# Optimization experiments

Hardware: AMD Instinct MI355X
Metric: run time of the kernel (lower is better)

## Reference

```python
import jax, jax.numpy as jnp
import numpy as np

D_MODEL = 512
N_HEAD = 8
D_HEAD = 64
N_LAYER = 4
D_INNER = 2048
IN_CH = 2048
N_CLS = 64
B, T = 2, 2048
LN_EPS = 1e-5


def layer_norm(x, s, b):
    mu = jnp.mean(x, axis=-1, keepdims=True)
    var = jnp.mean(jnp.square(x - mu), axis=-1, keepdims=True)
    return (x - mu) * jax.lax.rsqrt(var + LN_EPS) * s + b


def rel_shift(x):
    # x: [q, k, b, n] -> Transformer-XL relative shift
    q, k, b, n = x.shape
    zp = jnp.zeros((q, 1, b, n), x.dtype)
    x = jnp.concatenate([zp, x], axis=1)          # [q, k+1, b, n]
    x = x.reshape(k + 1, q, b, n)[1:]             # drop first row
    return x.reshape(q, k, b, n)


def setup_inputs() -> dict:
    key = jax.random.key(0)
    ks = jax.random.split(key, 12)
    s = 0.02
    return {
        "x": jax.random.normal(ks[0], (B, IN_CH, T), jnp.float32),
        "emb_w": jax.random.normal(ks[1], (D_MODEL, IN_CH), jnp.float32) * s,
        "emb_b": jnp.zeros((D_MODEL,), jnp.float32),
        "r_w_bias": jax.random.normal(ks[2], (N_HEAD, D_HEAD), jnp.float32) * s,
        "r_r_bias": jax.random.normal(ks[3], (N_HEAD, D_HEAD), jnp.float32) * s,
        "qkv_w": jax.random.normal(ks[4], (N_LAYER, 3 * N_HEAD * D_HEAD, D_MODEL), jnp.float32) * s,
        "qkv_b": jnp.zeros((N_LAYER, 3 * N_HEAD * D_HEAD), jnp.float32),
        "r_proj_w": jax.random.normal(ks[5], (N_LAYER, N_HEAD * D_HEAD, D_MODEL), jnp.float32) * s,
        "o_w": jax.random.normal(ks[6], (N_LAYER, D_MODEL, N_HEAD * D_HEAD), jnp.float32) * s,
        "ln1_s": jnp.ones((N_LAYER, D_MODEL), jnp.float32),
        "ln1_b": jnp.zeros((N_LAYER, D_MODEL), jnp.float32),
        "ff1_w": jax.random.normal(ks[7], (N_LAYER, D_INNER, D_MODEL), jnp.float32) * s,
        "ff1_b": jnp.zeros((N_LAYER, D_INNER), jnp.float32),
        "ff2_w": jax.random.normal(ks[8], (N_LAYER, D_MODEL, D_INNER), jnp.float32) * s,
        "ff2_b": jnp.zeros((N_LAYER, D_MODEL), jnp.float32),
        "ln2_s": jnp.ones((N_LAYER, D_MODEL), jnp.float32),
        "ln2_b": jnp.zeros((N_LAYER, D_MODEL), jnp.float32),
        "cls_w": jax.random.normal(ks[9], (N_CLS, D_MODEL), jnp.float32) * s,
        "cls_b": jnp.zeros((N_CLS,), jnp.float32),
    }


def reference(x, emb_w, emb_b, r_w_bias, r_r_bias, qkv_w, qkv_b, r_proj_w, o_w,
              ln1_s, ln1_b, ff1_w, ff1_b, ff2_w, ff2_b, ln2_s, ln2_b, cls_w, cls_b):
    b, _, t = x.shape
    d = D_MODEL
    # 1x1 conv embedding, then to [T, B, d_model] layout as in _forward
    h = jnp.einsum('dc,bct->tbd', emb_w, x) + emb_b

    # sinusoidal positional embedding over pos_seq = klen-1 .. 0 (klen == qlen, mem_len=0)
    pos_seq = jnp.arange(t - 1, -1, -1, dtype=h.dtype)
    inv_freq = 1.0 / (10000.0 ** (jnp.arange(0, d, 2, dtype=h.dtype) / d))
    sinusoid = pos_seq[:, None] * inv_freq[None, :]
    pos_emb = jnp.concatenate([jnp.sin(sinusoid), jnp.cos(sinusoid)], axis=-1)  # [T, d]

    scale = 1.0 / (D_HEAD ** 0.5)
    for i in range(N_LAYER):
        w = h
        heads = jnp.einsum('ed,tbd->tbe', qkv_w[i], w) + qkv_b[i]          # [T,B,3*H*Dh]
        q, k, v = jnp.split(heads, 3, axis=-1)
        q = q.reshape(t, b, N_HEAD, D_HEAD)
        k = k.reshape(t, b, N_HEAD, D_HEAD)
        v = v.reshape(t, b, N_HEAD, D_HEAD)
        r_head_k = jnp.einsum('ed,td->te', r_proj_w[i], pos_emb).reshape(t, N_HEAD, D_HEAD)

        AC = jnp.einsum('ibnd,jbnd->ijbn', q + r_w_bias, k)                # content term
        BD = rel_shift(jnp.einsum('ibnd,jnd->ijbn', q + r_r_bias, r_head_k))  # position term
        attn_prob = jax.nn.softmax((AC + BD) * scale, axis=1)              # softmax over keys
        attn_vec = jnp.einsum('ijbn,jbnd->ibnd', attn_prob, v).reshape(t, b, N_HEAD * D_HEAD)
        attn_out = jnp.einsum('de,tbe->tbd', o_w[i], attn_vec)             # o_net (no bias)
        h = layer_norm(w + attn_out, ln1_s[i], ln1_b[i])                   # post-lnorm

        ff = jnp.einsum('fd,tbd->tbf', ff1_w[i], h) + ff1_b[i]
        ff = jax.nn.relu(ff)
        ff = jnp.einsum('df,tbf->tbd', ff2_w[i], ff) + ff2_b[i]
        h = layer_norm(h + ff, ln2_s[i], ln2_b[i])

    # 1x1 conv classifier -> [B, num_classes, T]
    out = jnp.einsum('kd,tbd->bkt', cls_w, h) + cls_b[None, :, None]
    return out
```

## Files before the change

### kernel.cpp

```cpp
#include <hip/hip_runtime.h>
#include <hip/hip_bf16.h>
#include <math.h>


#define T_   2048
#define B_   2
#define DM   512
#define NH   8
#define DH   64
#define DI   2048
#define INCH 2048
#define NCLS 64
#define MT   4096

typedef __attribute__((ext_vector_type(8))) short short8;
typedef __attribute__((ext_vector_type(4))) float float4v;

#define QSCALE 0.1803368801111204f

__device__ inline ushort f2bf(float f) {
  uint u = __float_as_uint(f);
  return (ushort)((u + 0x7FFFu + ((u >> 16) & 1u)) >> 16);
}
__device__ inline float bf2f(ushort h) { return __uint_as_float(((uint)h) << 16); }
__device__ inline uint pkbf(float a, float b) {
  __hip_bfloat162 h = __float22bfloat162_rn(float2{a, b});
  return *(uint*)&h;
}
__device__ inline void gload16(const void* g, void* lds) {
  __builtin_amdgcn_global_load_lds(
      (const __attribute__((address_space(1))) void*)g,
      (__attribute__((address_space(3))) void*)lds, 16, 0, 0);
}

__global__ __launch_bounds__(256) void pos_kernel(ushort* __restrict__ pe) {
  int idx = blockIdx.x * 256 + threadIdx.x;
  if (idx >= T_ * DM) return;
  int t = idx >> 9;
  int i = idx & 511;
  int j = (i < 256) ? i : (i - 256);
  double invf = exp(-(double)(2 * j) * (9.210340371976184 / 512.0));
  double a = (double)(T_ - 1 - t) * invf;
  pe[idx] = f2bf((i < 256) ? (float)sin(a) : (float)cos(a));
}

__global__ __launch_bounds__(256) void cvt6_kernel(
    const float* s0, ushort* d0, int n0,
    const float* s1, ushort* d1, int n1,
    const float* s2, ushort* d2, int n2,
    const float* s3, ushort* d3, int n3,
    const float* s4, ushort* d4, int n4,
    const float* s5, ushort* d5, int n5)
{
  const float* s; ushort* d; int n;
  switch (blockIdx.y) {
    case 0: s = s0; d = d0; n = n0; break;
    case 1: s = s1; d = d1; n = n1; break;
    case 2: s = s2; d = d2; n = n2; break;
    case 3: s = s3; d = d3; n = n3; break;
    case 4: s = s4; d = d4; n = n4; break;
    default: s = s5; d = d5; n = n5; break;
  }
  int i = blockIdx.x * 256 + threadIdx.x;
  if (i >= n) return;
  float4 v = ((const float4*)s)[i];
  ushort4 w = { f2bf(v.x), f2bf(v.y), f2bf(v.z), f2bf(v.w) };
  ((ushort4*)d)[i] = w;
}

__global__ __launch_bounds__(256) void xpose_kernel(const float* __restrict__ x,
                                                    ushort* __restrict__ xb) {
  __shared__ float s[32][33];
  int t0 = blockIdx.x * 32, k0 = blockIdx.y * 32, b = blockIdx.z;
  int tx = threadIdx.x & 31, ty = threadIdx.x >> 5;
#pragma unroll
  for (int l = 0; l < 4; ++l) {
    int k = k0 + ty + l * 8;
    s[ty + l * 8][tx] = x[((size_t)b * INCH + k) * T_ + t0 + tx];
  }
  __syncthreads();
#pragma unroll
  for (int l = 0; l < 4; ++l) {
    int t = t0 + ty + l * 8;
    xb[((size_t)(t * 2 + b)) * INCH + k0 + tx] = f2bf(s[tx][ty + l * 8]);
  }
}

__global__ __launch_bounds__(256) void vtrans_kernel(const ushort* __restrict__ heads,
                                                     ushort* __restrict__ vtg) {
  __shared__ ushort s[64][72];
  const int tid = threadIdx.x;
  int t0 = blockIdx.x * 64;
  int b = blockIdx.y & 1, n = blockIdx.y >> 1;
  for (int e = tid; e < 512; e += 256) {
    int r = e >> 3, c = e & 7;
    *(uint4*)&s[r][c * 8] =
        *(const uint4*)&heads[(size_t)((t0 + r) * 2 + b) * 1536 + 1024 + n * 64 + c * 8];
  }
  __syncthreads();
  for (int e = tid; e < 512; e += 256) {
    int d = e >> 3, c = e & 7;
    ushort tmp[8];
#pragma unroll
    for (int j = 0; j < 8; ++j) tmp[j] = s[c * 8 + j][d];
    *(uint4*)&vtg[((size_t)((b * 8 + n) * 64 + d)) * (size_t)T_ + t0 + c * 8] = *(uint4*)tmp;
  }
}

template<int TM, int OUTMODE, bool RELU>
__global__ __launch_bounds__(256) void gemm_bf16(
    const ushort* __restrict__ A, const ushort* __restrict__ W,
    const float* __restrict__ bias, float* __restrict__ Cf, ushort* __restrict__ Cb,
    int M, int N, int K)
{
  __shared__ __attribute__((aligned(16))) ushort As[TM * 64];
  __shared__ __attribute__((aligned(16))) ushort Bs[128 * 64];
  const int NI = TM / 32;
  const int tid  = threadIdx.x;
  const int wave = tid >> 6, lane = tid & 63;
  const int quad = lane >> 4, lidx = lane & 15;
  const int m0 = blockIdx.y * TM, n0 = blockIdx.x * 128;
  const int r8 = lane >> 3;
  const int cs = ((lane & 7) ^ (r8 & 7)) * 8;

  float4v acc[NI * 4];
#pragma unroll
  for (int i = 0; i < NI * 4; ++i) acc[i] = (float4v){0.f, 0.f, 0.f, 0.f};

  const int wm = (wave >> 1) * (TM / 2), wn = (wave & 1) * 64;

  for (int k0 = 0; k0 < K; k0 += 64) {
    __syncthreads();
#pragma unroll
    for (int g = 0; g < TM / 32; ++g) {
      int r0 = wave * 8 + g * 32;
      gload16(A + (size_t)(m0 + r0 + r8) * K + k0 + cs, &As[r0 * 64]);
    }
#pragma unroll
    for (int g = 0; g < 4; ++g) {
      int r0 = wave * 8 + g * 32;
      gload16(W + (size_t)(n0 + r0 + r8) * K + k0 + cs, &Bs[r0 * 64]);
    }
    __syncthreads();

#pragma unroll
    for (int kb = 0; kb < 2; ++kb) {
      short8 af[NI], bf4[4];
      const int ch = (((kb * 4 + quad) ^ (lidx & 7)) * 8);
#pragma unroll
      for (int i = 0; i < NI; ++i)
        af[i] = *(const short8*)&As[(wm + i * 16 + lidx) * 64 + ch];
#pragma unroll
      for (int j = 0; j < 4; ++j)
        bf4[j] = *(const short8*)&Bs[(wn + j * 16 + lidx) * 64 + ch];
#pragma unroll
      for (int i = 0; i < NI; ++i)
#pragma unroll
        for (int j = 0; j < 4; ++j)
          acc[i * 4 + j] = __builtin_amdgcn_mfma_f32_16x16x32_bf16(af[i], bf4[j], acc[i * 4 + j], 0, 0, 0);
    }
  }

  float bj[4];
#pragma unroll
  for (int j = 0; j < 4; ++j) bj[j] = bias ? bias[n0 + wn + j * 16 + lidx] : 0.f;
#pragma unroll
  for (int i = 0; i < NI; ++i) {
    int rbase = m0 + wm + i * 16 + quad * 4;
#pragma unroll
    for (int j = 0; j < 4; ++j) {
      int col = n0 + wn + j * 16 + lidx;
#pragma unroll
      for (int reg = 0; reg < 4; ++reg) {
        float v = acc[i * 4 + j][reg] + bj[j];
        if (RELU) v = fmaxf(v, 0.f);
        size_t off = (size_t)(rbase + reg) * N + col;
        if (OUTMODE != 1) Cf[off] = v;
        if (OUTMODE != 0) Cb[off] = f2bf(v);
      }
    }
  }
}

#define BM 128
#define BN 128
#define BK 16
#define LDT 132

__global__ __launch_bounds__(256) void gemm_f32(
    const float* __restrict__ A, const float* __restrict__ W,
    const float* __restrict__ bias, float* __restrict__ C,
    int M, int N, int K)
{
  __shared__ float Asm[BK][LDT];
  __shared__ float Wsm[BK][LDT];
  const int tid = threadIdx.x;
  const int m0 = blockIdx.y * BM;
  const int n0 = blockIdx.x * BN;
  const int row = tid >> 1;
  const int kh  = (tid & 1) * 8;
  const int ty  = tid >> 4;
  const int tx  = tid & 15;

  float acc[8][8];
#pragma unroll
  for (int i = 0; i < 8; ++i)
#pragma unroll
    for (int j = 0; j < 8; ++j) acc[i][j] = 0.f;

  for (int kt = 0; kt < K; kt += BK) {
    float a_reg[8], w_reg[8];
    {
      const float* ap = A + (size_t)(m0 + row) * K + (kt + kh);
      float4 v0 = *(const float4*)ap;
      float4 v1 = *(const float4*)(ap + 4);
      a_reg[0] = v0.x; a_reg[1] = v0.y; a_reg[2] = v0.z; a_reg[3] = v0.w;
      a_reg[4] = v1.x; a_reg[5] = v1.y; a_reg[6] = v1.z; a_reg[7] = v1.w;
    }
    {
      int nn = n0 + row;
      if (nn < N) {
        const float* wp = W + (size_t)nn * K + (kt + kh);
        float4 v0 = *(const float4*)wp;
        float4 v1 = *(const float4*)(wp + 4);
        w_reg[0] = v0.x; w_reg[1] = v0.y; w_reg[2] = v0.z; w_reg[3] = v0.w;
        w_reg[4] = v1.x; w_reg[5] = v1.y; w_reg[6] = v1.z; w_reg[7] = v1.w;
      } else {
#pragma unroll
        for (int q = 0; q < 8; ++q) w_reg[q] = 0.f;
      }
    }
    __syncthreads();
#pragma unroll
    for (int q = 0; q < 8; ++q) { Asm[kh + q][row] = a_reg[q]; Wsm[kh + q][row] = w_reg[q]; }
    __syncthreads();
#pragma unroll
    for (int k = 0; k < BK; ++k) {
      float4 a0 = *(const float4*)&Asm[k][ty * 4];
      float4 a1 = *(const float4*)&Asm[k][ty * 4 + 64];
      float4 b0 = *(const float4*)&Wsm[k][tx * 4];
      float4 b1 = *(const float4*)&Wsm[k][tx * 4 + 64];
      float av[8] = {a0.x, a0.y, a0.z, a0.w, a1.x, a1.y, a1.z, a1.w};
      float bv[8] = {b0.x, b0.y, b0.z, b0.w, b1.x, b1.y, b1.z, b1.w};
#pragma unroll
      for (int i = 0; i < 8; ++i)
#pragma unroll
        for (int j = 0; j < 8; ++j) acc[i][j] += av[i] * bv[j];
    }
  }

#pragma unroll
  for (int ih = 0; ih < 2; ++ih)
#pragma unroll
    for (int i = 0; i < 4; ++i) {
      int m = m0 + ty * 4 + ih * 64 + i;
#pragma unroll
      for (int jh = 0; jh < 2; ++jh) {
        int nn = n0 + tx * 4 + jh * 64;
        if (nn < N) {
          float4 v;
          v.x = acc[ih * 4 + i][jh * 4 + 0] + bias[nn + 0];
          v.y = acc[ih * 4 + i][jh * 4 + 1] + bias[nn + 1];
          v.z = acc[ih * 4 + i][jh * 4 + 2] + bias[nn + 2];
          v.w = acc[ih * 4 + i][jh * 4 + 3] + bias[nn + 3];
          *(float4*)&C[(size_t)m * N + nn] = v;
        }
      }
    }
}

#define GT 68

__device__ inline short8 bfrag(const char* base, int lidx, int quad, int kb) {
  return *(const short8*)(base + lidx * 128 + ((((kb << 2) + quad) ^ (lidx & 7)) << 4));
}

__global__ __launch_bounds__(256, 2) void attn_mfma_kernel(
    const ushort* __restrict__ heads, const ushort* __restrict__ rk,
    const ushort* __restrict__ vtg,
    const float* __restrict__ rwb, const float* __restrict__ rrb,
    ushort* __restrict__ avec)
{
  __shared__ __attribute__((aligned(16))) ushort Ks[64 * 64];
  __shared__ __attribute__((aligned(16))) ushort Vt[64 * 64];
  __shared__ __attribute__((aligned(16))) ushort Re[128 * 64];
  __shared__ __attribute__((aligned(16))) ushort Gbt[128 * GT];

  const int tid  = threadIdx.x;
  const int i0   = blockIdx.x * 64;
  const int b    = blockIdx.y & 1;
  const int n    = blockIdx.y >> 1;
  const int wave = tid >> 6;
  const int lane = tid & 63;
  const int quad = lane >> 4;
  const int lidx = lane & 15;
  const int r8   = lane >> 3;
  const int cs8  = ((lane & 7) ^ (r8 & 7)) * 8;
  const int bn64 = (b * 8 + n) * 64;
  const int rloc = wave * 16 + lidx;

  short8 qw[2], qr4[4][2], q4[2];
  {
    auto qfrag = [&](int row, int kb, const float* bias) -> short8 {
      short8 q;
      if (row < T_) q = *(const short8*)&heads[(size_t)(row * 2 + b) * 1536 + n * 64 + kb * 32 + quad * 8];
      else { for (int t = 0; t < 8; ++t) ((ushort*)&q)[t] = 0; }
      short8 o;
#pragma unroll
      for (int t = 0; t < 8; ++t) {
        float f = (bf2f((ushort)((ushort*)&q)[t]) + bias[n * 64 + kb * 32 + quad * 8 + t]) * QSCALE;
        ((ushort*)&o)[t] = f2bf(f);
      }
      return o;
    };
    qw[0] = qfrag(i0 + rloc, 0, rwb);
    qw[1] = qfrag(i0 + rloc, 1, rwb);
#pragma unroll
    for (int rt = 0; rt < 4; ++rt) {
      int row = i0 + rt * 16 + lidx;
      qr4[rt][0] = qfrag(row, 0, rrb); qr4[rt][1] = qfrag(row, 1, rrb);
    }
    int row4 = i0 + 64 + lidx;
    q4[0] = qfrag(row4, 0, rrb); q4[1] = qfrag(row4, 1, rrb);
  }

  int a0[4];
#pragma unroll
  for (int t = 0; t < 4; ++t)
    a0[t] = (t * 16 + quad * 4 + 63 - rloc) * GT + rloc;

  float4v oacc[4];
  float4v liacc = (float4v){0.f, 0.f, 0.f, 0.f};
#pragma unroll
  for (int dt = 0; dt < 4; ++dt) oacc[dt] = (float4v){0.f, 0.f, 0.f, 0.f};
  short8 ones8;
#pragma unroll
  for (int t = 0; t < 8; ++t) ((ushort*)&ones8)[t] = 0x3F80;

  auto stageKRe = [&](int jt) {
    int j0 = jt * 64, qmin = j0 + 1984 - i0;
#pragma unroll
    for (int half = 0; half < 2; ++half) {
      int r0 = 8 * wave + 32 * half;
      gload16(heads + (size_t)((j0 + r0 + r8) * 2 + b) * 1536 + 512 + n * 64 + cs8, &Ks[r0 * 64]);
    }
#pragma unroll
    for (int q4i = 0; q4i < 4; ++q4i) {
      int r0 = 8 * wave + 32 * q4i;
      int qh = qmin + r0 + r8;
      int p  = (qh > T_) ? (qh - T_ - 1) : ((qh == T_) ? 0 : qh);
      gload16(rk + (size_t)p * 2048 + n * 64 + cs8, &Re[r0 * 64]);
    }
  };
  auto stageV = [&](int jt) {
    int j0 = jt * 64;
#pragma unroll
    for (int half = 0; half < 2; ++half) {
      int r0 = 8 * wave + 32 * half;
      gload16(vtg + (size_t)(bn64 + r0 + r8) * (size_t)T_ + j0 + cs8, &Vt[r0 * 64]);
    }
  };
  auto fixup = [&](int jt) {
    int qmin = jt * 64 + 1984 - i0;
    int Tidx = T_ - qmin;
    if (Tidx >= 0 && Tidx < 128) {
      if (tid < 32) ((uint*)Re)[Tidx * 32 + tid] = 0u;
      __syncthreads();
    }
  };

  stageKRe(0);
  stageV(0);
  __syncthreads();
  fixup(0);

  for (int jt = 0; jt < 32; ++jt) {
    const int qmin = jt * 64 + 1984 - i0;
    const int wth  = T_ - qmin;

    float4v sv[4];
#pragma unroll
    for (int t = 0; t < 4; ++t) {
      const char* KsT = (const char*)Ks + t * 2048;
      short8 kf0 = bfrag(KsT, lidx, quad, 0);
      short8 kf1 = bfrag(KsT, lidx, quad, 1);
      float4v c = {0.f, 0.f, 0.f, 0.f};
      c = __builtin_amdgcn_mfma_f32_16x16x32_bf16(kf0, qw[0], c, 0, 0, 0);
      c = __builtin_amdgcn_mfma_f32_16x16x32_bf16(kf1, qw[1], c, 0, 0, 0);
      sv[t] = c;
    }

#pragma unroll
    for (int si = 0; si < 2; ++si) {
      const int ws = wave + si * 4;
      const int w0 = ws * 16;
      const char* ReW = (const char*)Re + w0 * 128;
      short8 rb0 = bfrag(ReW, lidx, quad, 0);
      short8 rb1 = bfrag(ReW, lidx, quad, 1);
#pragma unroll
      for (int rt = 0; rt < 4; ++rt) {
        bool need = si == 0 ? (rt >= 3 - wave) : (rt <= 3 - wave);
        if (need) {
          float4v g = {0.f, 0.f, 0.f, 0.f};
          g = __builtin_amdgcn_mfma_f32_16x16x32_bf16(qr4[rt][0], rb0, g, 0, 0, 0);
          g = __builtin_amdgcn_mfma_f32_16x16x32_bf16(qr4[rt][1], rb1, g, 0, 0, 0);
          uint2 st; st.x = pkbf(g[0], g[1]); st.y = pkbf(g[2], g[3]);
          *(uint2*)&Gbt[(w0 + lidx) * GT + rt * 16 + quad * 4] = st;
        }
      }
      if (si == 0 && wth < 63) {
        float4v g = {0.f, 0.f, 0.f, 0.f};
        g = __builtin_amdgcn_mfma_f32_16x16x32_bf16(q4[0], rb0, g, 0, 0, 0);
        g = __builtin_amdgcn_mfma_f32_16x16x32_bf16(q4[1], rb1, g, 0, 0, 0);
        if (quad == 0) Gbt[(w0 + lidx) * GT + 64] = f2bf(g[0]);
      }
    }
    __syncthreads();

    if (jt < 31) stageKRe(jt + 1);

    {
      const int cth = wth + rloc - 63;
#pragma unroll
      for (int t = 0; t < 4; ++t) {
        const int c0 = t * 16 + quad * 4;
#pragma unroll
        for (int r = 0; r < 4; ++r) {
          int ga = a0[t] + r * GT + ((c0 + r > cth) ? 1 : 0);
          sv[t][r] = exp2f(sv[t][r] + bf2f(Gbt[ga]));
        }
      }
    }

    short8 vb[4][2];
#pragma unroll
    for (int dt = 0; dt < 4; ++dt) {
      const char* VtT = (const char*)Vt + dt * 2048;
      vb[dt][0] = bfrag(VtT, lidx, quad, 0);
      vb[dt][1] = bfrag(VtT, lidx, quad, 1);
    }

    short8 af[2];
#pragma unroll
    for (int kb = 0; kb < 2; ++kb) {
      uint mm[4];
#pragma unroll
      for (int i = 0; i < 2; ++i) {
        uint e, o;
        asm("v_cvt_pk_bf16_f32 %0, %1, %2" : "=v"(e) : "v"(sv[2 * kb][2 * i]),     "v"(sv[2 * kb][2 * i + 1]));
        asm("v_cvt_pk_bf16_f32 %0, %1, %2" : "=v"(o) : "v"(sv[2 * kb + 1][2 * i]), "v"(sv[2 * kb + 1][2 * i + 1]));
        asm("v_permlane32_swap_b32 %0, %1" : "+v"(e), "+v"(o));
        asm("v_permlane16_swap_b32 %0, %1" : "+v"(e), "+v"(o));
        mm[i] = e; mm[2 + i] = o;
      }
      union { uint u[4]; short8 s; } cv;
      cv.u[0] = mm[0]; cv.u[1] = mm[1]; cv.u[2] = mm[2]; cv.u[3] = mm[3];
      af[kb] = cv.s;
    }

    __syncthreads();

    if (jt < 31) {
      stageV(jt + 1);
      fixup(jt + 1);
    }

#pragma unroll
    for (int dt = 0; dt < 4; ++dt) {
      oacc[dt] = __builtin_amdgcn_mfma_f32_16x16x32_bf16(af[0], vb[dt][0], oacc[dt], 0, 0, 0);
      oacc[dt] = __builtin_amdgcn_mfma_f32_16x16x32_bf16(af[1], vb[dt][1], oacc[dt], 0, 0, 0);
    }
    liacc = __builtin_amdgcn_mfma_f32_16x16x32_bf16(af[0], ones8, liacc, 0, 0, 0);
    liacc = __builtin_amdgcn_mfma_f32_16x16x32_bf16(af[1], ones8, liacc, 0, 0, 0);
  }

#pragma unroll
  for (int reg = 0; reg < 4; ++reg) {
    int i = i0 + wave * 16 + quad * 4 + reg;
    float li = liacc[reg];
#pragma unroll
    for (int dt = 0; dt < 4; ++dt) {
      float val = oacc[dt][reg] / li;
      avec[(size_t)(i * 2 + b) * DM + n * 64 + dt * 16 + lidx] = f2bf(val);
    }
  }
}

__global__ __launch_bounds__(256) void ln_res_kernel(
    float* __restrict__ h, ushort* __restrict__ hb, const float* __restrict__ delta,
    const float* __restrict__ s, const float* __restrict__ bb)
{
  const int m = blockIdx.x;
  const int tid = threadIdx.x;
  float* hp = h + (size_t)m * DM;
  ushort* hbp = hb + (size_t)m * DM;
  const float* dp = delta + (size_t)m * DM;
  float x0 = hp[tid] + dp[tid];
  float x1 = hp[tid + 256] + dp[tid + 256];
  float sum = x0 + x1, sq = x0 * x0 + x1 * x1;
#pragma unroll
  for (int o = 32; o > 0; o >>= 1) { sum += __shfl_down(sum, o); sq += __shfl_down(sq, o); }
  __shared__ float part[8];
  int wv = tid >> 6;
  if ((tid & 63) == 0) { part[wv * 2] = sum; part[wv * 2 + 1] = sq; }
  __syncthreads();
  float ts = part[0] + part[2] + part[4] + part[6];
  float tq = part[1] + part[3] + part[5] + part[7];
  float mu = ts * (1.f / DM);
  float var = tq * (1.f / DM) - mu * mu;
  float rs = rsqrtf(var + 1e-5f);
  float y0 = (x0 - mu) * rs * s[tid]       + bb[tid];
  float y1 = (x1 - mu) * rs * s[tid + 256] + bb[tid + 256];
  hp[tid] = y0;       hbp[tid] = f2bf(y0);
  hp[tid + 256] = y1; hbp[tid + 256] = f2bf(y1);
}

__global__ __launch_bounds__(256) void reorder_kernel(const float* __restrict__ ct,
                                                      float* __restrict__ out) {
  int idx = blockIdx.x * 256 + threadIdx.x;
  if (idx >= B_ * NCLS * T_) return;
  int t  = idx & (T_ - 1);
  int nc = (idx >> 11) & 63;
  int bb = idx >> 17;
  out[idx] = ct[(size_t)(t * B_ + bb) * NCLS + nc];
}

extern "C" void kernel_launch(void* const* d_in, const int* in_sizes, int n_in,
                              void* d_out, int out_size, void* d_ws, size_t ws_size,
                              hipStream_t stream)
{
  const float* x     = (const float*)d_in[0];
  const float* emb_w = (const float*)d_in[1];
  const float* emb_b = (const float*)d_in[2];
  const float* rwb   = (const float*)d_in[3];
  const float* rrb   = (const float*)d_in[4];
  const float* qkv_w = (const float*)d_in[5];
  const float* qkv_b = (const float*)d_in[6];
  const float* rproj = (const float*)d_in[7];
  const float* o_w   = (const float*)d_in[8];
  const float* ln1s  = (const float*)d_in[9];
  const float* ln1b  = (const float*)d_in[10];
  const float* ff1w  = (const float*)d_in[11];
  const float* ff1b  = (const float*)d_in[12];
  const float* ff2w  = (const float*)d_in[13];
  const float* ff2b  = (const float*)d_in[14];
  const float* ln2s  = (const float*)d_in[15];
  const float* ln2b  = (const float*)d_in[16];
  const float* clsw  = (const float*)d_in[17];
  const float* clsb  = (const float*)d_in[18];
  float* out = (float*)d_out;

  char* p = (char*)d_ws;
  float*  h       = (float*)p;   p += (size_t)MT * DM * 4;
  float*  tmpf    = (float*)p;   p += (size_t)MT * DM * 4;
  ushort* hb      = (ushort*)p;  p += (size_t)MT * DM * 2;
  ushort* headsb  = (ushort*)p;  p += (size_t)MT * 1536 * 2;
  ushort* peb     = (ushort*)p;  p += (size_t)T_ * DM * 2;
  ushort* rk_all  = (ushort*)p;  p += (size_t)T_ * 2048 * 2;
  ushort* avecb   = (ushort*)p;  p += (size_t)MT * DM * 2;
  ushort* xfb     = (ushort*)p;  p += (size_t)MT * INCH * 2;
  ushort* emb_wb  = (ushort*)p;  p += (size_t)DM * INCH * 2;
  ushort* qkv_wb  = (ushort*)p;  p += (size_t)4 * 1536 * DM * 2;
  ushort* rproj_wb= (ushort*)p;  p += (size_t)4 * DM * DM * 2;
  ushort* o_wb    = (ushort*)p;  p += (size_t)4 * DM * DM * 2;
  ushort* ff1_wb  = (ushort*)p;  p += (size_t)4 * DI * DM * 2;
  ushort* ff2_wb  = (ushort*)p;  p += (size_t)4 * DM * DI * 2;
  ushort* vtg     = xfb;

  cvt6_kernel<<<dim3(4096, 6), 256, 0, stream>>>(
      emb_w, emb_wb, DM * INCH / 4,
      qkv_w, qkv_wb, 4 * 1536 * DM / 4,
      rproj, rproj_wb, 4 * DM * DM / 4,
      o_w,   o_wb,   4 * DM * DM / 4,
      ff1w,  ff1_wb, 4 * DI * DM / 4,
      ff2w,  ff2_wb, 4 * DM * DI / 4);
  pos_kernel<<<(T_ * DM) / 256, 256, 0, stream>>>(peb);
  xpose_kernel<<<dim3(T_ / 32, INCH / 32, B_), 256, 0, stream>>>(x, xfb);

  gemm_bf16<64, 2, false><<<dim3(DM / 128, MT / 64), 256, 0, stream>>>(
      xfb, emb_wb, emb_b, h, hb, MT, DM, INCH);
  gemm_bf16<128, 1, false><<<dim3(2048 / 128, T_ / 128), 256, 0, stream>>>(
      peb, rproj_wb, nullptr, nullptr, rk_all, T_, 2048, DM);

  for (int l = 0; l < 4; ++l) {
    gemm_bf16<128, 1, false><<<dim3(1536 / 128, MT / 128), 256, 0, stream>>>(
        hb, qkv_wb + (size_t)l * 1536 * DM, qkv_b + l * 1536, nullptr, headsb, MT, 1536, DM);
    vtrans_kernel<<<dim3(T_ / 64, B_ * NH), 256, 0, stream>>>(headsb, vtg);
    attn_mfma_kernel<<<dim3(T_ / 64, B_ * NH), 256, 0, stream>>>(
        headsb, rk_all + (size_t)l * 512, vtg, rwb, rrb, avecb);
    gemm_bf16<32, 0, false><<<dim3(DM / 128, MT / 32), 256, 0, stream>>>(
        avecb, o_wb + (size_t)l * DM * DM, nullptr, tmpf, nullptr, MT, DM, DM);
    ln_res_kernel<<<MT, 256, 0, stream>>>(h, hb, tmpf, ln1s + l * DM, ln1b + l * DM);
    gemm_bf16<128, 1, true><<<dim3(DI / 128, MT / 128), 256, 0, stream>>>(
        hb, ff1_wb + (size_t)l * DI * DM, ff1b + l * DI, nullptr, xfb, MT, DI, DM);
    gemm_bf16<32, 0, false><<<dim3(DM / 128, MT / 32), 256, 0, stream>>>(
        xfb, ff2_wb + (size_t)l * DM * DI, ff2b + l * DM, tmpf, nullptr, MT, DM, DI);
    ln_res_kernel<<<MT, 256, 0, stream>>>(h, hb, tmpf, ln2s + l * DM, ln2b + l * DM);
  }

  gemm_f32<<<dim3(1, MT / BM), 256, 0, stream>>>(h, clsw, clsb, tmpf, MT, NCLS, DM);
  reorder_kernel<<<(B_ * NCLS * T_) / 256, 256, 0, stream>>>(tmpf, out);
}
```

Baseline: 925.3 us.

## Split attention over key chunks with atomic accumulation and a normalize pass

Splits the attention key loop into three chunks along a new grid dimension, so each block does about a third of the key tiles. Partial numerators and denominators go to float buffers with atomicAdd, and a separate kernel then normalizes and writes bf16 output. The aim is more concurrent blocks, since the old grid had only 512 blocks. It also raises the occupancy hint to 3 and uses the hardware exp2 builtin. In exchange it adds a zeroing kernel, atomic traffic and an extra pass, and the sum order is no longer deterministic. That is safe only because the softmax has no running max; it uses plain exp with a fixed scale.

```diff
diff --git a/kernel.cpp b/kernel.cpp
--- a/kernel.cpp
+++ b/kernel.cpp
@@ -275,11 +275,11 @@
   return *(const short8*)(base + lidx * 128 + ((((kb << 2) + quad) ^ (lidx & 7)) << 4));
 }
 
-__global__ __launch_bounds__(256, 2) void attn_mfma_kernel(
+__global__ __launch_bounds__(256, 3) void attn_mfma_kernel(
     const ushort* __restrict__ heads, const ushort* __restrict__ rk,
     const ushort* __restrict__ vtg,
     const float* __restrict__ rwb, const float* __restrict__ rrb,
-    ushort* __restrict__ avec)
+    float* __restrict__ Oacc, float* __restrict__ Lg)
 {
   __shared__ __attribute__((aligned(16))) ushort Ks[64 * 64];
   __shared__ __attribute__((aligned(16))) ushort Vt[64 * 64];
@@ -290,6 +290,9 @@
   const int i0   = blockIdx.x * 64;
   const int b    = blockIdx.y & 1;
   const int n    = blockIdx.y >> 1;
+  const int chunk = blockIdx.z;
+  const int jt0 = (chunk == 0) ? 0  : (chunk == 1 ? 11 : 22);
+  const int jt1 = (chunk == 0) ? 11 : (chunk == 1 ? 22 : 32);
   const int wave = tid >> 6;
   const int lane = tid & 63;
   const int quad = lane >> 4;
@@ -369,12 +372,12 @@
     }
   };
 
-  stageKRe(0);
-  stageV(0);
+  stageKRe(jt0);
+  stageV(jt0);
   __syncthreads();
-  fixup(0);
-
-  for (int jt = 0; jt < 32; ++jt) {
+  fixup(jt0);
+
+  for (int jt = jt0; jt < jt1; ++jt) {
     const int qmin = jt * 64 + 1984 - i0;
     const int wth  = T_ - qmin;
 
@@ -417,7 +420,7 @@
     }
     __syncthreads();
 
-    if (jt < 31) stageKRe(jt + 1);
+    if (jt + 1 < jt1) stageKRe(jt + 1);
 
     {
       const int cth = wth + rloc - 63;
@@ -427,7 +430,7 @@
 #pragma unroll
         for (int r = 0; r < 4; ++r) {
           int ga = a0[t] + r * GT + ((c0 + r > cth) ? 1 : 0);
-          sv[t][r] = exp2f(sv[t][r] + bf2f(Gbt[ga]));
+          sv[t][r] = __builtin_amdgcn_exp2f(sv[t][r] + bf2f(Gbt[ga]));
         }
       }
     }
@@ -460,7 +463,7 @@
 
     __syncthreads();
 
-    if (jt < 31) {
+    if (jt + 1 < jt1) {
       stageV(jt + 1);
       fixup(jt + 1);
     }
@@ -474,16 +477,37 @@
     liacc = __builtin_amdgcn_mfma_f32_16x16x32_bf16(af[1], ones8, liacc, 0, 0, 0);
   }
 
+  const int rowg0 = (b * 8 + n) * T_ + i0 + wave * 16 + quad * 4;
 #pragma unroll
   for (int reg = 0; reg < 4; ++reg) {
-    int i = i0 + wave * 16 + quad * 4 + reg;
-    float li = liacc[reg];
-#pragma unroll
-    for (int dt = 0; dt < 4; ++dt) {
-      float val = oacc[dt][reg] / li;
-      avec[(size_t)(i * 2 + b) * DM + n * 64 + dt * 16 + lidx] = f2bf(val);
-    }
-  }
+    int rowg = rowg0 + reg;
+#pragma unroll
+    for (int dt = 0; dt < 4; ++dt)
+      atomicAdd(&Oacc[(size_t)rowg * 64 + dt * 16 + lidx], oacc[dt][reg]);
+    if (lidx == 0) atomicAdd(&Lg[rowg], liacc[reg]);
+  }
+}
+
+__global__ __launch_bounds__(256) void zero2_kernel(float4* __restrict__ a, int na,
+                                                    float4* __restrict__ b2, int nb) {
+  int i = blockIdx.x * 256 + threadIdx.x;
+  if (i < na) a[i] = float4{0.f, 0.f, 0.f, 0.f};
+  int j = i - na;
+  if (j >= 0 && j < nb) b2[j] = float4{0.f, 0.f, 0.f, 0.f};
+}
+
+__global__ __launch_bounds__(256) void attn_norm_kernel(const float* __restrict__ Oacc,
+                                                        const float* __restrict__ Lg,
+                                                        ushort* __restrict__ avec) {
+  int idx = blockIdx.x * 256 + threadIdx.x;
+  int d4  = idx & 15;
+  int row = (idx >> 4) & 2047;
+  int bn  = idx >> 15;
+  float4 v = ((const float4*)Oacc)[idx];
+  float inv = 1.0f / Lg[(bn << 11) + row];
+  int b = bn >> 3, n = bn & 7;
+  ushort4 w = { f2bf(v.x * inv), f2bf(v.y * inv), f2bf(v.z * inv), f2bf(v.w * inv) };
+  *(ushort4*)&avec[(size_t)(row * 2 + b) * DM + n * 64 + d4 * 4] = w;
 }
 
 __global__ __launch_bounds__(256) void ln_res_kernel(
@@ -565,6 +589,7 @@
   ushort* o_wb    = (ushort*)p;  p += (size_t)4 * DM * DM * 2;
   ushort* ff1_wb  = (ushort*)p;  p += (size_t)4 * DI * DM * 2;
   ushort* ff2_wb  = (ushort*)p;  p += (size_t)4 * DM * DI * 2;
+  float*  Lg      = (float*)p;   p += (size_t)16 * T_ * 4;
   ushort* vtg     = xfb;
 
   cvt6_kernel<<<dim3(4096, 6), 256, 0, stream>>>(
@@ -582,12 +607,18 @@
   gemm_bf16<128, 1, false><<<dim3(2048 / 128, T_ / 128), 256, 0, stream>>>(
       peb, rproj_wb, nullptr, nullptr, rk_all, T_, 2048, DM);
 
+  const int NO4 = MT * DM / 4;
+  const int NL4 = 16 * T_ / 4;
+
   for (int l = 0; l < 4; ++l) {
     gemm_bf16<128, 1, false><<<dim3(1536 / 128, MT / 128), 256, 0, stream>>>(
         hb, qkv_wb + (size_t)l * 1536 * DM, qkv_b + l * 1536, nullptr, headsb, MT, 1536, DM);
     vtrans_kernel<<<dim3(T_ / 64, B_ * NH), 256, 0, stream>>>(headsb, vtg);
-    attn_mfma_kernel<<<dim3(T_ / 64, B_ * NH), 256, 0, stream>>>(
-        headsb, rk_all + (size_t)l * 512, vtg, rwb, rrb, avecb);
+    zero2_kernel<<<(NO4 + NL4 + 255) / 256, 256, 0, stream>>>(
+        (float4*)tmpf, NO4, (float4*)Lg, NL4);
+    attn_mfma_kernel<<<dim3(T_ / 64, B_ * NH, 3), 256, 0, stream>>>(
+        headsb, rk_all + (size_t)l * 512, vtg, rwb, rrb, tmpf, Lg);
+    attn_norm_kernel<<<(16 * T_ * 16) / 256, 256, 0, stream>>>(tmpf, Lg, avecb);
     gemm_bf16<32, 0, false><<<dim3(DM / 128, MT / 32), 256, 0, stream>>>(
         avecb, o_wb + (size_t)l * DM * DM, nullptr, tmpf, nullptr, MT, DM, DM);
     ln_res_kernel<<<MT, 256, 0, stream>>>(h, hb, tmpf, ln1s + l * DM, ln1b + l * DM);
```

After: 944.5 us. +2.1%, slower.
